# Performance work log

Measured on AMD Instinct MI355X. Metric: run time of the kernel, lower is better.

The kernel has to match this reference:

```python
import jax
import jax.numpy as jnp
from jax import lax
import numpy as np

N_NODES = 1_000_000
DEGREE = 31            # neighbors per agent -> group_size = DEGREE + 1
GROUP = DEGREE + 1
THRESHOLD = 16         # CRD threshold M = group_size / 2
COST = 0.25            # CRD cooperation cost c


def setup_inputs() -> dict:
    key = jax.random.key(0)
    k1, k2 = jax.random.split(key)
    gains = jax.random.normal(k1, (N_NODES,), dtype=jnp.float32)
    neighbors = jax.random.randint(k2, (N_NODES, DEGREE), 0, N_NODES, dtype=jnp.int64)
    return {"gains": gains, "neighbors": neighbors}


def reference(gains, neighbors):
    # sigmoid cooperation prob per agent, then neighbor gather -> [N, GROUP]
    p = jax.nn.sigmoid(gains)                       # [N]
    group_p = jnp.concatenate([p[:, None], p[neighbors]], axis=1)  # [N, GROUP]

    # Poisson-Binomial PMF via DP convolution over group members.
    # dp[n, k] = P(k cooperators among members processed so far)
    n = group_p.shape[0]
    dp0 = jnp.zeros((n, GROUP + 1), dtype=group_p.dtype).at[:, 0].set(1.0)

    def step(dp, pj):  # pj: [N] coop prob of one group member
        pj = pj[:, None]
        shifted = jnp.pad(dp[:, :-1], ((0, 0), (1, 0)))  # dp shifted by one success
        return dp * (1.0 - pj) + shifted * pj, None

    dp, _ = lax.scan(step, dp0, group_p.T)          # scan over GROUP members

    prob_above = dp[:, THRESHOLD:].sum(axis=1)      # P(count >= THRESHOLD), [N]
    acum_loss = jnp.sum(prob_above - COST * p)
    return -acum_loss
```

## Files before the change

### kernel.cpp

```cpp
#include <hip/hip_runtime.h>

constexpr int DEG = 31;
constexpr int NEV = 32;
constexpr int TH  = 16;
constexpr int BLK = 256;
constexpr int TBL = 1 << 20;

typedef int  vint4  __attribute__((ext_vector_type(4)));

__global__ void zero_out_kernel(float* out) {
    if (threadIdx.x == 0) out[0] = 0.0f;
}

__device__ __forceinline__ float fast_sigmoid(float x) {
    return 1.0f / (1.0f + __expf(-x));
}

__global__ __launch_bounds__(256)
void build_table_kernel(const float* __restrict__ gains,
                        unsigned* __restrict__ tbl4,
                        float* __restrict__ out, int n) {
    const int t = blockIdx.x * 256 + threadIdx.x;
    if (t == 0) out[0] = 0.0f;
    if (t < TBL / 4) {
        unsigned w = 0;
        #pragma unroll
        for (int k = 0; k < 4; ++k) {
            const int i = 4 * t + k;
            const float p = (i < n) ? fast_sigmoid(gains[i]) : 0.0f;
            const unsigned b = __float2uint_rn(p * 255.0f);
            w |= (b & 0xFFu) << (8 * k);
        }
        tbl4[t] = w;
    }
}

__global__ __launch_bounds__(BLK, 5)
void pgl_kernel(const float* __restrict__ gains,
                const int*   __restrict__ nbr,
                const unsigned char* __restrict__ tbl,
                float*       __restrict__ out, int n) {
    __shared__ int s_idx[BLK * DEG];
    __shared__ float s_red[BLK / 64];

    const int tid        = threadIdx.x;
    const int blockStart = blockIdx.x * BLK;

    const int rows  = min(BLK, n - blockStart);
    const int elems = rows * DEG;
    const int base  = blockStart * DEG;
    {
        const vint4* nb4 = (const vint4*)(nbr + base);
        vint4*       s4  = (vint4*)s_idx;
        const int nvec   = elems >> 2;
        for (int v = tid; v < nvec; v += BLK)
            s4[v] = __builtin_nontemporal_load(nb4 + v);
        for (int e = (nvec << 2) + tid; e < elems; e += BLK)
            s_idx[e] = __builtin_nontemporal_load(nbr + base + e);
    }
    __syncthreads();

    float local = 0.0f;
    const int i = blockStart + tid;
    if (i < n) {
        const int* row = s_idx + tid * DEG;

        unsigned idxs[DEG];
        #pragma unroll
        for (int j = 0; j < DEG; ++j) idxs[j] = (unsigned)row[j];

        const float g0 = __builtin_nontemporal_load(gains + i);

        unsigned gb[DEG];
        #pragma unroll
        for (int j = 0; j < DEG; ++j) {
            gb[j] = __hip_atomic_load(tbl + idxs[j],
                                      __ATOMIC_RELAXED,
                                      __HIP_MEMORY_SCOPE_AGENT);
        }

        __builtin_amdgcn_sched_barrier(0);

        const float p0 = fast_sigmoid(g0);

        float dp[TH];
        dp[0] = 1.0f;
        #pragma unroll
        for (int k = 1; k < TH; ++k) dp[k] = 0.0f;
        float over = 0.0f;

        #pragma unroll
        for (int j = 0; j < NEV; ++j) {
            const float pj = (j == 0) ? p0 : (float)gb[j - 1] * (1.0f / 255.0f);
            if (j >= TH - 1) over = fmaf(dp[TH - 1], pj, over);
            const int kmax = (j + 1 < TH - 1) ? (j + 1) : (TH - 1);
            #pragma unroll
            for (int k = kmax; k >= 1; --k)
                dp[k] = fmaf(pj, dp[k - 1] - dp[k], dp[k]);
            dp[0] = fmaf(-pj, dp[0], dp[0]);
        }
        local = fmaf(0.25f, p0, -over);
    }

    #pragma unroll
    for (int o = 32; o > 0; o >>= 1) local += __shfl_down(local, o, 64);
    if ((tid & 63) == 0) s_red[tid >> 6] = local;
    __syncthreads();
    if (tid == 0) {
        float s = 0.0f;
        #pragma unroll
        for (int w = 0; w < BLK / 64; ++w) s += s_red[w];
        atomicAdd(out, s);
    }
}

__global__ __launch_bounds__(BLK)
void pgl_direct_kernel(const float* __restrict__ gains,
                       const int*   __restrict__ nbr,
                       float*       __restrict__ out, int n) {
    __shared__ int s_idx[BLK * DEG];
    __shared__ float s_red[BLK / 64];
    const int tid = threadIdx.x;
    const int blockStart = blockIdx.x * BLK;
    const int rows  = min(BLK, n - blockStart);
    const int elems = rows * DEG;
    const int base  = blockStart * DEG;
    const int4* nb4 = (const int4*)(nbr + base);
    int4* s4 = (int4*)s_idx;
    const int nvec = elems >> 2;
    for (int v = tid; v < nvec; v += BLK) s4[v] = nb4[v];
    for (int e = (nvec << 2) + tid; e < elems; e += BLK) s_idx[e] = nbr[base + e];
    __syncthreads();
    float local = 0.0f;
    const int i = blockStart + tid;
    if (i < n) {
        const int* row = s_idx + tid * DEG;
        float dp[TH];
        dp[0] = 1.0f;
        #pragma unroll
        for (int k = 1; k < TH; ++k) dp[k] = 0.0f;
        float over = 0.0f;
        const float p0 = fast_sigmoid(gains[i]);
        #pragma unroll
        for (int j = 0; j < NEV; ++j) {
            const float pj = (j == 0) ? p0 : fast_sigmoid(gains[row[j - 1]]);
            if (j >= TH - 1) over = fmaf(dp[TH - 1], pj, over);
            const int kmax = (j + 1 < TH - 1) ? (j + 1) : (TH - 1);
            #pragma unroll
            for (int k = kmax; k >= 1; --k)
                dp[k] = fmaf(pj, dp[k - 1] - dp[k], dp[k]);
            dp[0] = fmaf(-pj, dp[0], dp[0]);
        }
        local = fmaf(0.25f, p0, -over);
    }
    #pragma unroll
    for (int o = 32; o > 0; o >>= 1) local += __shfl_down(local, o, 64);
    if ((tid & 63) == 0) s_red[tid >> 6] = local;
    __syncthreads();
    if (tid == 0) {
        float s = 0.0f;
        #pragma unroll
        for (int w = 0; w < BLK / 64; ++w) s += s_red[w];
        atomicAdd(out, s);
    }
}

extern "C" void kernel_launch(void* const* d_in, const int* in_sizes, int n_in,
                              void* d_out, int out_size, void* d_ws, size_t ws_size,
                              hipStream_t stream) {
    const float* gains = (const float*)d_in[0];
    const int*   nbr   = (const int*)d_in[1];
    float*       out   = (float*)d_out;
    const int n = in_sizes[0];

    const int grid = (n + BLK - 1) / BLK;
    if (ws_size >= (size_t)TBL && n <= TBL) {
        unsigned char* tbl = (unsigned char*)d_ws;
        build_table_kernel<<<(TBL / 4 + 255) / 256, 256, 0, stream>>>(
            gains, (unsigned*)tbl, out, n);
        pgl_kernel<<<grid, BLK, 0, stream>>>(gains, nbr, tbl, out, n);
    } else {
        zero_out_kernel<<<1, 64, 0, stream>>>(out);
        pgl_direct_kernel<<<grid, BLK, 0, stream>>>(gains, nbr, out, n);
    }
}
```

Baseline: 293.3 us.

## Gather table bytes via chunked LDS scan instead of random global loads

Each 1024-thread block handles 2048 nodes, keeps their neighbor indices in registers, and streams the 1MB byte table through 64KB of shared memory in 16 passes. Each thread picks out the neighbor bytes that fall in the current chunk. This replaces scattered global byte gathers with coalesced table loads and LDS reads. The cost is that every block re-reads the whole table, does many predicated LDS lookups, and runs at lower occupancy because of the large LDS footprint.

```diff
diff --git a/kernel.cpp b/kernel.cpp
--- a/kernel.cpp
+++ b/kernel.cpp
@@ -5,6 +5,11 @@
 constexpr int TH  = 16;
 constexpr int BLK = 256;
 constexpr int TBL = 1 << 20;
+
+constexpr int CH    = 1 << 16;
+constexpr int NPASS = TBL / CH;
+constexpr int BLK2  = 1024;
+constexpr int NPB   = 2048;
 
 typedef int  vint4  __attribute__((ext_vector_type(4)));
 
@@ -35,81 +40,118 @@
     }
 }
 
-__global__ __launch_bounds__(BLK, 5)
-void pgl_kernel(const float* __restrict__ gains,
-                const int*   __restrict__ nbr,
-                const unsigned char* __restrict__ tbl,
-                float*       __restrict__ out, int n) {
-    __shared__ int s_idx[BLK * DEG];
-    __shared__ float s_red[BLK / 64];
+__device__ __forceinline__ float node_dp(float g, const unsigned w[8]) {
+    const float p0 = fast_sigmoid(g);
+    float dp[TH];
+    dp[0] = 1.0f;
+    #pragma unroll
+    for (int k = 1; k < TH; ++k) dp[k] = 0.0f;
+    float over = 0.0f;
+    #pragma unroll
+    for (int j = 0; j < NEV; ++j) {
+        float pj;
+        if (j == 0) {
+            pj = p0;
+        } else {
+            const unsigned b = (w[(j - 1) >> 2] >> (((j - 1) & 3) * 8)) & 0xFFu;
+            pj = (float)b * (1.0f / 255.0f);
+        }
+        if (j >= TH - 1) over = fmaf(dp[TH - 1], pj, over);
+        const int kmax = (j + 1 < TH - 1) ? (j + 1) : (TH - 1);
+        #pragma unroll
+        for (int k = kmax; k >= 1; --k)
+            dp[k] = fmaf(pj, dp[k - 1] - dp[k], dp[k]);
+        dp[0] = fmaf(-pj, dp[0], dp[0]);
+    }
+    return fmaf(0.25f, p0, -over);
+}
+
+__global__ __launch_bounds__(BLK2, 4)
+void pgl2_kernel(const float* __restrict__ gains,
+                 const int*   __restrict__ nbr,
+                 const unsigned char* __restrict__ tbl,
+                 float*       __restrict__ out, int n) {
+    __shared__ __align__(16) unsigned char smem[CH];
 
     const int tid        = threadIdx.x;
-    const int blockStart = blockIdx.x * BLK;
-
-    const int rows  = min(BLK, n - blockStart);
-    const int elems = rows * DEG;
-    const int base  = blockStart * DEG;
-    {
+    const int blockStart = blockIdx.x * NPB;
+    const int rows_total = min(NPB, n - blockStart);
+
+    unsigned idxA[DEG], idxB[DEG];
+    #pragma unroll
+    for (int j = 0; j < DEG; ++j) { idxA[j] = 0u; idxB[j] = 0u; }
+
+    #pragma unroll
+    for (int r = 0; r < 4; ++r) {
+        const int rowsR = max(0, min(512, rows_total - r * 512));
+        const int elems = rowsR * DEG;
+        const int base  = (blockStart + r * 512) * DEG;
         const vint4* nb4 = (const vint4*)(nbr + base);
-        vint4*       s4  = (vint4*)s_idx;
-        const int nvec   = elems >> 2;
-        for (int v = tid; v < nvec; v += BLK)
+        vint4* s4 = (vint4*)smem;
+        const int nvec = elems >> 2;
+        for (int v = tid; v < nvec; v += BLK2)
             s4[v] = __builtin_nontemporal_load(nb4 + v);
-        for (int e = (nvec << 2) + tid; e < elems; e += BLK)
-            s_idx[e] = __builtin_nontemporal_load(nbr + base + e);
-    }
-    __syncthreads();
+        for (int e = (nvec << 2) + tid; e < elems; e += BLK2)
+            ((int*)smem)[e] = __builtin_nontemporal_load(nbr + base + e);
+        __syncthreads();
+        const int half = r & 1;
+        const int s    = tid - half * 512;
+        if (s >= 0 && s < rowsR) {
+            const int* row = (const int*)smem + s * DEG;
+            if ((r >> 1) == 0) {
+                #pragma unroll
+                for (int j = 0; j < DEG; ++j) idxA[j] = (unsigned)row[j];
+            } else {
+                #pragma unroll
+                for (int j = 0; j < DEG; ++j) idxB[j] = (unsigned)row[j];
+            }
+        }
+        __syncthreads();
+    }
+
+    unsigned wA[8], wB[8];
+    #pragma unroll
+    for (int q = 0; q < 8; ++q) { wA[q] = 0u; wB[q] = 0u; }
+
+    #pragma unroll 1
+    for (int c = 0; c < NPASS; ++c) {
+        {
+            const vint4* t4 = (const vint4*)(tbl + (size_t)c * CH);
+            vint4* s4 = (vint4*)smem;
+            #pragma unroll
+            for (int q = 0; q < CH / 16 / BLK2; ++q)
+                s4[q * BLK2 + tid] = t4[q * BLK2 + tid];
+        }
+        __syncthreads();
+
+        const unsigned base = (unsigned)c * (unsigned)CH;
+        #pragma unroll
+        for (int j = 0; j < DEG; ++j) {
+            const unsigned rA = idxA[j] - base;
+            if (rA < (unsigned)CH)
+                wA[j >> 2] |= (unsigned)smem[rA] << ((j & 3) * 8);
+            const unsigned rB = idxB[j] - base;
+            if (rB < (unsigned)CH)
+                wB[j >> 2] |= (unsigned)smem[rB] << ((j & 3) * 8);
+        }
+        __syncthreads();
+    }
 
     float local = 0.0f;
-    const int i = blockStart + tid;
-    if (i < n) {
-        const int* row = s_idx + tid * DEG;
-
-        unsigned idxs[DEG];
-        #pragma unroll
-        for (int j = 0; j < DEG; ++j) idxs[j] = (unsigned)row[j];
-
-        const float g0 = __builtin_nontemporal_load(gains + i);
-
-        unsigned gb[DEG];
-        #pragma unroll
-        for (int j = 0; j < DEG; ++j) {
-            gb[j] = __hip_atomic_load(tbl + idxs[j],
-                                      __ATOMIC_RELAXED,
-                                      __HIP_MEMORY_SCOPE_AGENT);
-        }
-
-        __builtin_amdgcn_sched_barrier(0);
-
-        const float p0 = fast_sigmoid(g0);
-
-        float dp[TH];
-        dp[0] = 1.0f;
-        #pragma unroll
-        for (int k = 1; k < TH; ++k) dp[k] = 0.0f;
-        float over = 0.0f;
-
-        #pragma unroll
-        for (int j = 0; j < NEV; ++j) {
-            const float pj = (j == 0) ? p0 : (float)gb[j - 1] * (1.0f / 255.0f);
-            if (j >= TH - 1) over = fmaf(dp[TH - 1], pj, over);
-            const int kmax = (j + 1 < TH - 1) ? (j + 1) : (TH - 1);
-            #pragma unroll
-            for (int k = kmax; k >= 1; --k)
-                dp[k] = fmaf(pj, dp[k - 1] - dp[k], dp[k]);
-            dp[0] = fmaf(-pj, dp[0], dp[0]);
-        }
-        local = fmaf(0.25f, p0, -over);
-    }
+    const int iA = blockStart + tid;
+    const int iB = blockStart + 1024 + tid;
+    if (iA < n) local += node_dp(__builtin_nontemporal_load(gains + iA), wA);
+    if (iB < n) local += node_dp(__builtin_nontemporal_load(gains + iB), wB);
 
     #pragma unroll
     for (int o = 32; o > 0; o >>= 1) local += __shfl_down(local, o, 64);
+    float* s_red = (float*)smem;
     if ((tid & 63) == 0) s_red[tid >> 6] = local;
     __syncthreads();
     if (tid == 0) {
         float s = 0.0f;
         #pragma unroll
-        for (int w = 0; w < BLK / 64; ++w) s += s_red[w];
+        for (int w = 0; w < BLK2 / 64; ++w) s += s_red[w];
         atomicAdd(out, s);
     }
 }
@@ -173,14 +215,15 @@
     float*       out   = (float*)d_out;
     const int n = in_sizes[0];
 
-    const int grid = (n + BLK - 1) / BLK;
     if (ws_size >= (size_t)TBL && n <= TBL) {
         unsigned char* tbl = (unsigned char*)d_ws;
         build_table_kernel<<<(TBL / 4 + 255) / 256, 256, 0, stream>>>(
             gains, (unsigned*)tbl, out, n);
-        pgl_kernel<<<grid, BLK, 0, stream>>>(gains, nbr, tbl, out, n);
+        const int grid2 = (n + NPB - 1) / NPB;
+        pgl2_kernel<<<grid2, BLK2, 0, stream>>>(gains, nbr, tbl, out, n);
     } else {
         zero_out_kernel<<<1, 64, 0, stream>>>(out);
+        const int grid = (n + BLK - 1) / BLK;
         pgl_direct_kernel<<<grid, BLK, 0, stream>>>(gains, nbr, out, n);
     }
 }
```

New measurement: 305.9 us. 4.3% more time.
